# Performance work log

Measured on AMD Instinct MI355X. Metric: run time of the kernel, lower is better.

The kernel has to match this reference:

```python
import jax, jax.numpy as jnp
import numpy as np

B, N, H = 32, 2048, 128
L4H = 4 * H  # concatenated (c0,h0,c1,h1) embedding dim


def _lstm_cell(x, c, h, Wx, Wh, b):
    g = x @ Wx + h @ Wh + b                      # [B,N,4H]
    i, f, gg, o = jnp.split(g, 4, axis=-1)
    c_new = jax.nn.sigmoid(f) * c + jax.nn.sigmoid(i) * jnp.tanh(gg)
    h_new = jax.nn.sigmoid(o) * jnp.tanh(c_new)
    return c_new, h_new


def setup_inputs() -> dict:
    key = jax.random.key(0)
    ks = jax.random.split(key, 20)
    s = 0.05
    inp = {
        'node_embeddings': jax.random.normal(ks[0], (B, N, H), jnp.float32),
        'c0': jax.random.normal(ks[1], (B, N, H), jnp.float32),
        'h0': jax.random.normal(ks[2], (B, N, H), jnp.float32),
        'c1': jax.random.normal(ks[3], (B, N, H), jnp.float32),
        'h1': jax.random.normal(ks[4], (B, N, H), jnp.float32),
        'instruction_pointer': jax.random.uniform(ks[5], (B, N), jnp.float32),
        'Wx0': s * jax.random.normal(ks[6], (H, 4 * H), jnp.float32),
        'Wh0': s * jax.random.normal(ks[7], (H, 4 * H), jnp.float32),
        'b0': jnp.zeros((4 * H,), jnp.float32),
        'Wx1': s * jax.random.normal(ks[8], (H, 4 * H), jnp.float32),
        'Wh1': s * jax.random.normal(ks[9], (H, 4 * H), jnp.float32),
        'b1': jnp.zeros((4 * H,), jnp.float32),
        'raise_W': s * jax.random.normal(ks[10], (L4H, 2), jnp.float32),
        'raise_b': jnp.zeros((2,), jnp.float32),
        'branch_W': s * jax.random.normal(ks[11], (L4H, 2), jnp.float32),
        'branch_b': jnp.zeros((2,), jnp.float32),
        'true_indexes': jax.random.randint(ks[12], (B, N), 0, N, jnp.int32),
        'false_indexes': jax.random.randint(ks[13], (B, N), 0, N, jnp.int32),
        'raise_indexes': jax.random.randint(ks[14], (B, N), 0, N, jnp.int32),
        'exit_node_indexes': jax.random.randint(ks[15], (B,), 0, N, jnp.int32),
        'raise_node_indexes': jax.random.randint(ks[16], (B,), 0, N, jnp.int32),
        'current_step': jnp.zeros((B,), jnp.int32),
        'step_limits': jax.random.randint(ks[17], (B,), 1, 100, jnp.int32),
    }
    return inp


def reference(node_embeddings, c0, h0, c1, h1, instruction_pointer,
              Wx0, Wh0, b0, Wx1, Wh1, b1, raise_W, raise_b, branch_W, branch_b,
              true_indexes, false_indexes, raise_indexes,
              exit_node_indexes, raise_node_indexes, current_step, step_limits):
    num_nodes = node_embeddings.shape[1]

    # --- execute: stacked 2-layer LSTM per node (vectorized over B,N) ---
    c0n, h0n = _lstm_cell(node_embeddings, c0, h0, Wx0, Wh0, b0)
    c1n, h1n = _lstm_cell(h0n, c1, h1, Wx1, Wh1, b1)
    old = (c0, h0, c1, h1)
    contrib = (c0n, h0n, c1n, h1n)

    # --- mask exit and raise nodes: keep old hidden state there ---
    node_ids = jnp.arange(num_nodes)[None, :]                  # [1,N]
    m_exit = node_ids == exit_node_indexes[:, None]            # [B,N]
    m_raise = node_ids == raise_node_indexes[:, None]          # [B,N]
    m_keep = (m_exit | m_raise)[..., None]                     # raise_in_ipagnn=True
    contrib = tuple(jnp.where(m_keep, o, c) for o, c in zip(old, contrib))

    # --- raise / branch decisions ---
    emb = jnp.concatenate(contrib, axis=-1)                    # [B,N,4H]
    raise_dec = jax.nn.softmax(emb @ raise_W + raise_b, axis=-1)
    raise_dec = jnp.where(m_exit[..., None], jnp.array([0.0, 1.0], raise_dec.dtype), raise_dec)
    branch_dec = jax.nn.softmax(emb @ branch_W + branch_b, axis=-1)

    p_raise = raise_dec[..., 0]
    p_noraise = raise_dec[..., 1]
    p_true = p_noraise * branch_dec[..., 0]
    p_false = p_noraise * branch_dec[..., 1]

    seg = jax.vmap(lambda d, i: jax.ops.segment_sum(d, i, num_segments=num_nodes))

    # --- instruction pointer update (scatter-add over soft edges) ---
    ip = instruction_pointer
    ip_new = (seg(p_raise * ip, raise_indexes)
              + seg(p_true * ip, true_indexes)
              + seg(p_false * ip, false_indexes))               # [B,N]

    # --- hidden-state aggregation, weighted by instruction pointer ---
    denom = (ip_new + 1e-7)[..., None]                          # [B,N,1]
    wr = (p_raise * ip)[..., None]
    wt = (p_true * ip)[..., None]
    wf = (p_false * ip)[..., None]
    agg = tuple((seg(hc * wr, raise_indexes)
                 + seg(hc * wt, true_indexes)
                 + seg(hc * wf, false_indexes)) / denom
                for hc in contrib)

    # --- keep old state if example already hit its step limit ---
    live = (current_step < step_limits)                         # [B]
    ip_fin = jnp.where(live[:, None], ip_new, ip)
    hid_fin = tuple(jnp.where(live[:, None, None], a, o) for a, o in zip(agg, old))

    # pack carry: (c0,h0,c1,h1) embedding + instruction pointer -> [B,N,4H+1]
    return jnp.concatenate(list(hid_fin) + [ip_fin[..., None]], axis=-1)
```

## Files before the change

kernel.cpp:

```cpp
#include <hip/hip_runtime.h>
#include <hip/hip_bf16.h>

constexpr int Bc  = 32;
constexpr int Nc  = 2048;
constexpr int Hc  = 128;
constexpr int H4c = 512;
constexpr int BNc = Bc * Nc;

typedef __attribute__((ext_vector_type(8))) short short8;
typedef __attribute__((ext_vector_type(4))) float f32x4;

__device__ __forceinline__ float sigf(float x)  { return 1.f / (1.f + __expf(-x)); }
__device__ __forceinline__ float tanh_(float x) { return 1.f - 2.f / (__expf(2.f * x) + 1.f); }

__device__ __forceinline__ unsigned short bfu(float f) {
    union { float f; unsigned u; } a; a.f = f;
    unsigned u = a.u;
    return (unsigned short)((u + 0x7FFFu + ((u >> 16) & 1u)) >> 16);
}
__device__ __forceinline__ float bf2f(unsigned short u) {
    union { unsigned u; float f; } a; a.u = ((unsigned)u) << 16;
    return a.f;
}
__device__ __forceinline__ unsigned cvtpk(float lo, float hi) {
    unsigned r;
    asm("v_cvt_pk_bf16_f32 %0, %1, %2" : "=v"(r) : "v"(lo), "v"(hi));
    return r;
}

__device__ __forceinline__ int a_off(int buf, int row, int byte) {
    return buf * 5120 + row * 80 + byte;
}
__device__ __forceinline__ int cs_off(int row, int unit) {
    return row * 512 + ((unit ^ (row & 7)) << 4);
}

__global__ __launch_bounds__(256) void prep_kernel(
    const float* __restrict__ Wx0, const float* __restrict__ Wh0,
    const float* __restrict__ Wx1, const float* __restrict__ Wh1,
    unsigned short* __restrict__ W0F, unsigned short* __restrict__ W1F)
{
    int idx = blockIdx.x * 256 + threadIdx.x;
    int ct = idx >> 9, ks = (idx >> 6) & 7, lane = idx & 63;
    int col = ct * 16 + (lane & 15);
    unsigned short* p0 = W0F + (size_t)idx * 8;
    unsigned short* p1 = W1F + (size_t)idx * 8;
    #pragma unroll
    for (int e = 0; e < 8; ++e) {
        int k = ks * 32 + (lane >> 4) * 8 + e;
        float v0 = (k < 128) ? Wx0[k * 512 + col] : Wh0[(k - 128) * 512 + col];
        float v1 = (k < 128) ? Wx1[k * 512 + col] : Wh1[(k - 128) * 512 + col];
        p0[e] = bfu(v0);
        p1[e] = bfu(v1);
    }
}

__global__ __launch_bounds__(512, 4) void gemm0_kernel(
    const float* __restrict__ x_in,  const float* __restrict__ c0_in,
    const float* __restrict__ h0_in,
    const unsigned short* __restrict__ W0F, const float* __restrict__ b0,
    const int* __restrict__ exit_i, const int* __restrict__ raise_i,
    unsigned short* __restrict__ contrib)
{
    __shared__ __align__(16) char Ab[10240];
    __shared__ __align__(16) char Cs[32768];

    const int t    = threadIdx.x;
    const int w    = t >> 6, l = t & 63, lr = l & 15, lg = l >> 4;
    const int row0 = blockIdx.x * 64;
    const int bidx = row0 >> 11;
    const int eb   = exit_i[bidx];
    const int rbn  = raise_i[bidx];
    const int j    = w * 16 + lr;

    const int srow = t >> 3, sfq = t & 7;
#define STAGE0(c, bi)                                                          \
    {                                                                          \
        const float* sp = ((c) < 4 ? x_in : h0_in)                             \
            + (size_t)(row0 + srow) * Hc + ((c) & 3) * 32 + sfq * 4;           \
        float4 v = *(const float4*)sp;                                         \
        uint2 b2 = { cvtpk(v.x, v.y), cvtpk(v.z, v.w) };                       \
        *(uint2*)(Ab + a_off(bi, srow, sfq * 8)) = b2;                         \
    }

    f32x4 acc[4][4];
    #pragma unroll
    for (int g = 0; g < 4; ++g) {
        float bv = b0[g * 128 + j];
        f32x4 vv = {bv, bv, bv, bv};
        #pragma unroll
        for (int mt = 0; mt < 4; ++mt) acc[mt][g] = vv;
    }

    STAGE0(0, 0);
    short8 bn[4];
    #pragma unroll
    for (int g = 0; g < 4; ++g)
        bn[g] = *(const short8*)(W0F + ((size_t)((g * 8 + w) * 8) * 64 + l) * 8);
    #pragma unroll
    for (int c = 0; c < 8; ++c) {
        __syncthreads();
        short8 bc[4];
        #pragma unroll
        for (int g = 0; g < 4; ++g) bc[g] = bn[g];
        if (c < 7) {
            STAGE0(c + 1, (c + 1) & 1);
            #pragma unroll
            for (int g = 0; g < 4; ++g)
                bn[g] = *(const short8*)(W0F + ((size_t)((g * 8 + w) * 8 + c + 1) * 64 + l) * 8);
        }
        short8 a[4];
        #pragma unroll
        for (int mt = 0; mt < 4; ++mt)
            a[mt] = *(const short8*)(Ab + a_off(c & 1, mt * 16 + lr, lg * 16));
        #pragma unroll
        for (int mt = 0; mt < 4; ++mt)
            #pragma unroll
            for (int g = 0; g < 4; ++g)
                acc[mt][g] = __builtin_amdgcn_mfma_f32_16x16x32_bf16(
                    a[mt], bc[g], acc[mt][g], 0, 0, 0);
    }

    #pragma unroll
    for (int mt = 0; mt < 4; ++mt) {
        #pragma unroll
        for (int rr = 0; rr < 4; ++rr) {
            const int row  = mt * 16 + lg * 4 + rr;
            const int grow = row0 + row;
            const int n    = grow & (Nc - 1);
            float cold = c0_in[(size_t)grow * Hc + j];
            float ig = sigf(acc[mt][0][rr]);
            float fg = sigf(acc[mt][1][rr]);
            float gv = tanh_(acc[mt][2][rr]);
            float og = sigf(acc[mt][3][rr]);
            float cn = fg * cold + ig * gv;
            float hn = og * tanh_(cn);
            const bool keep = (n == eb) || (n == rbn);
            float cw = keep ? cold : cn;
            float hw = hn;
            if (keep) hw = h0_in[(size_t)grow * Hc + j];
            *(unsigned short*)(Cs + cs_off(row, j >> 3) + (j & 7) * 2)        = bfu(cw);
            *(unsigned short*)(Cs + cs_off(row, 16 + (j >> 3)) + (j & 7) * 2) = bfu(hw);
        }
    }
    __syncthreads();
    #pragma unroll
    for (int i = 0; i < 4; ++i) {
        const int idx = i * 512 + t;
        const int r = idx >> 5, u = idx & 31;
        short8 v = *(const short8*)(Cs + cs_off(r, u));
        *(short8*)(contrib + (size_t)(row0 + r) * H4c + u * 8) = v;
    }
#undef STAGE0
}

__global__ __launch_bounds__(512, 4) void gemm1_kernel(
    const unsigned short* __restrict__ contrib_r, const float* __restrict__ c1_in,
    const float* __restrict__ h1_in,
    const unsigned short* __restrict__ W1F, const float* __restrict__ b1,
    const float* __restrict__ rW, const float* __restrict__ rbv,
    const float* __restrict__ bW, const float* __restrict__ bbv,
    const float* __restrict__ ip_in,
    const int* __restrict__ exit_i, const int* __restrict__ raise_i,
    unsigned short* __restrict__ contrib, float* __restrict__ w_all)
{
    __shared__ __align__(16) char Ab[10240];
    __shared__ __align__(16) char Cs[32768];

    const int t    = threadIdx.x;
    const int w    = t >> 6, l = t & 63, lr = l & 15, lg = l >> 4;
    const int row0 = blockIdx.x * 64;
    const int bidx = row0 >> 11;
    const int eb   = exit_i[bidx];
    const int rbn  = raise_i[bidx];
    const int j    = w * 16 + lr;

    const int srow = t >> 3, sfq = t & 7;
#define STAGE1(c, bi)                                                          \
    {                                                                          \
        if ((c) < 4) {                                                         \
            ushort4 v = *(const ushort4*)(contrib_r                            \
                + (size_t)(row0 + srow) * H4c + 128 + ((c) & 3) * 32 + sfq * 4); \
            *(ushort4*)(Ab + a_off(bi, srow, sfq * 8)) = v;                    \
        } else {                                                               \
            const float* sp = h1_in + (size_t)(row0 + srow) * Hc               \
                + ((c) & 3) * 32 + sfq * 4;                                    \
            float4 v = *(const float4*)sp;                                     \
            uint2 b2 = { cvtpk(v.x, v.y), cvtpk(v.z, v.w) };                   \
            *(uint2*)(Ab + a_off(bi, srow, sfq * 8)) = b2;                     \
        }                                                                      \
    }

    f32x4 acc[4][4];
    #pragma unroll
    for (int g = 0; g < 4; ++g) {
        float bv = b1[g * 128 + j];
        f32x4 vv = {bv, bv, bv, bv};
        #pragma unroll
        for (int mt = 0; mt < 4; ++mt) acc[mt][g] = vv;
    }

    STAGE1(0, 0);
    short8 bn[4];
    #pragma unroll
    for (int g = 0; g < 4; ++g)
        bn[g] = *(const short8*)(W1F + ((size_t)((g * 8 + w) * 8) * 64 + l) * 8);
    #pragma unroll
    for (int c = 0; c < 8; ++c) {
        __syncthreads();
        short8 bc[4];
        #pragma unroll
        for (int g = 0; g < 4; ++g) bc[g] = bn[g];
        if (c < 7) {
            STAGE1(c + 1, (c + 1) & 1);
            #pragma unroll
            for (int g = 0; g < 4; ++g)
                bn[g] = *(const short8*)(W1F + ((size_t)((g * 8 + w) * 8 + c + 1) * 64 + l) * 8);
        }
        short8 a[4];
        #pragma unroll
        for (int mt = 0; mt < 4; ++mt)
            a[mt] = *(const short8*)(Ab + a_off(c & 1, mt * 16 + lr, lg * 16));
        #pragma unroll
        for (int mt = 0; mt < 4; ++mt)
            #pragma unroll
            for (int g = 0; g < 4; ++g)
                acc[mt][g] = __builtin_amdgcn_mfma_f32_16x16x32_bf16(
                    a[mt], bc[g], acc[mt][g], 0, 0, 0);
    }

    #pragma unroll
    for (int mt = 0; mt < 4; ++mt) {
        #pragma unroll
        for (int rr = 0; rr < 4; ++rr) {
            const int row  = mt * 16 + lg * 4 + rr;
            const int grow = row0 + row;
            const int n    = grow & (Nc - 1);
            float cold = c1_in[(size_t)grow * Hc + j];
            float ig = sigf(acc[mt][0][rr]);
            float fg = sigf(acc[mt][1][rr]);
            float gv = tanh_(acc[mt][2][rr]);
            float og = sigf(acc[mt][3][rr]);
            float cn = fg * cold + ig * gv;
            float hn = og * tanh_(cn);
            const bool keep = (n == eb) || (n == rbn);
            float cw = keep ? cold : cn;
            float hw = hn;
            if (keep) hw = h1_in[(size_t)grow * Hc + j];
            *(unsigned short*)(Cs + cs_off(row, j >> 3) + (j & 7) * 2)        = bfu(cw);
            *(unsigned short*)(Cs + cs_off(row, 16 + (j >> 3)) + (j & 7) * 2) = bfu(hw);
        }
    }
    __syncthreads();
    float* dw = (float*)Ab;
    if (t < 256) {
        ((float4*)dw)[t]       = ((const float4*)rW)[t];
        ((float4*)dw)[256 + t] = ((const float4*)bW)[t];
    }
    __syncthreads();
    #pragma unroll
    for (int i = 0; i < 4; ++i) {
        const int idx = i * 512 + t;
        const int r = idx >> 5, u = idx & 31;
        short8 v = *(const short8*)(Cs + cs_off(r, u));
        *(short8*)(contrib + (size_t)(row0 + r) * H4c + 256 + u * 8) = v;
    }

    {
        const int r8 = l >> 3, s = l & 7;
        const int row  = w * 8 + r8;
        const int grow = row0 + row;
        float pr0 = 0.f, pr1 = 0.f, pb0 = 0.f, pb1 = 0.f;
        #pragma unroll
        for (int cu = 0; cu < 8; ++cu) {
            short8 ev;
            if (s < 4)
                ev = *(const short8*)(contrib_r + (size_t)grow * H4c + s * 64 + cu * 8);
            else
                ev = *(const short8*)(Cs + cs_off(row, (s - 4) * 8 + cu));
            const int col0 = s * 64 + cu * 8;
            const float4* rp = (const float4*)(dw + col0 * 2);
            const float4* bp = (const float4*)(dw + 1024 + col0 * 2);
            #pragma unroll
            for (int q = 0; q < 4; ++q) {
                float4 rv = rp[q], bv = bp[q];
                float e0 = bf2f((unsigned short)ev[q * 2]);
                float e1 = bf2f((unsigned short)ev[q * 2 + 1]);
                pr0 += e0 * rv.x + e1 * rv.z;
                pr1 += e0 * rv.y + e1 * rv.w;
                pb0 += e0 * bv.x + e1 * bv.z;
                pb1 += e0 * bv.y + e1 * bv.w;
            }
        }
        #pragma unroll
        for (int m = 1; m < 8; m <<= 1) {
            pr0 += __shfl_xor(pr0, m);
            pr1 += __shfl_xor(pr1, m);
            pb0 += __shfl_xor(pb0, m);
            pb1 += __shfl_xor(pb1, m);
        }
        if (s == 0) {
            const int n = grow & (Nc - 1);
            float r0v = pr0 + rbv[0], r1v = pr1 + rbv[1];
            float m  = fmaxf(r0v, r1v);
            float z0 = __expf(r0v - m), z1 = __expf(r1v - m);
            float inv = 1.f / (z0 + z1);
            float praise = z0 * inv, pno = z1 * inv;
            if (n == eb) { praise = 0.f; pno = 1.f; }
            float q0 = pb0 + bbv[0], q1 = pb1 + bbv[1];
            float mm = fmaxf(q0, q1);
            float y0 = __expf(q0 - mm), y1 = __expf(q1 - mm);
            float binv = 1.f / (y0 + y1);
            float ipv = ip_in[grow];
            w_all[grow]            = praise * ipv;
            w_all[BNc + grow]      = pno * y0 * binv * ipv;
            w_all[2 * BNc + grow]  = pno * y1 * binv * ipv;
        }
    }
#undef STAGE1
}

__global__ __launch_bounds__(256) void build_kernel(
    const int* __restrict__ t_idx, const int* __restrict__ f_idx,
    const int* __restrict__ r_idx, int* __restrict__ head, int* __restrict__ nxt)
{
    const int row  = blockIdx.x * 256 + threadIdx.x;
    const int base = (row >> 11) << 11;
    const int e0 = row * 4;
    int o;
    o = atomicExch(&head[base + r_idx[row]], e0);     nxt[e0]     = o;
    o = atomicExch(&head[base + t_idx[row]], e0 + 1); nxt[e0 + 1] = o;
    o = atomicExch(&head[base + f_idx[row]], e0 + 2); nxt[e0 + 2] = o;
}

__global__ __launch_bounds__(256) void gather_kernel(
    const unsigned short* __restrict__ contrib, const float* __restrict__ w_all,
    const int* __restrict__ head, const int* __restrict__ nxt,
    const float* __restrict__ c0_in, const float* __restrict__ h0_in,
    const float* __restrict__ c1_in, const float* __restrict__ h1_in,
    const float* __restrict__ ip_in,
    const int* __restrict__ cstep, const int* __restrict__ slim,
    float* __restrict__ out)
{
    const int gtid = blockIdx.x * 256 + threadIdx.x;
    const int wid  = gtid >> 6;
    const int l    = gtid & 63;
    const int bidx = wid >> 11;

    float acc[8] = {0.f, 0.f, 0.f, 0.f, 0.f, 0.f, 0.f, 0.f};
    float ipsum = 0.f;

    int e = head[wid];
    while (e >= 0) {
        const int src = e >> 2;
        const float w = w_all[(e & 3) * BNc + src];
        const unsigned short* crow = contrib + (size_t)src * 512;
        #pragma unroll
        for (int q = 0; q < 8; ++q) acc[q] += w * bf2f(crow[q * 64 + l]);
        ipsum += w;
        e = nxt[e];
    }

    const bool live = cstep[bidx] < slim[bidx];
    float* orow = out + (size_t)wid * 513;
    if (live) {
        const float inv = 1.f / (ipsum + 1e-7f);
        #pragma unroll
        for (int q = 0; q < 8; ++q) orow[q * 64 + l] = acc[q] * inv;
        if (l == 0) orow[512] = ipsum;
    } else {
        #pragma unroll
        for (int q = 0; q < 8; ++q) {
            const int off = (q & 1) * 64 + l;
            const float* p = (q >> 1) == 0 ? c0_in : (q >> 1) == 1 ? h0_in
                           : (q >> 1) == 2 ? c1_in : h1_in;
            orow[q * 64 + l] = p[(size_t)wid * Hc + off];
        }
        if (l == 0) orow[512] = ip_in[wid];
    }
}

extern "C" void kernel_launch(void* const* d_in, const int* in_sizes, int n_in,
                              void* d_out, int out_size, void* d_ws, size_t ws_size,
                              hipStream_t stream) {
    const float* x     = (const float*)d_in[0];
    const float* c0    = (const float*)d_in[1];
    const float* h0    = (const float*)d_in[2];
    const float* c1    = (const float*)d_in[3];
    const float* h1    = (const float*)d_in[4];
    const float* ip    = (const float*)d_in[5];
    const float* Wx0   = (const float*)d_in[6];
    const float* Wh0   = (const float*)d_in[7];
    const float* b0    = (const float*)d_in[8];
    const float* Wx1   = (const float*)d_in[9];
    const float* Wh1   = (const float*)d_in[10];
    const float* b1    = (const float*)d_in[11];
    const float* rW    = (const float*)d_in[12];
    const float* rb    = (const float*)d_in[13];
    const float* bW    = (const float*)d_in[14];
    const float* bb    = (const float*)d_in[15];
    const int* t_idx   = (const int*)d_in[16];
    const int* f_idx   = (const int*)d_in[17];
    const int* r_idx   = (const int*)d_in[18];
    const int* exit_i  = (const int*)d_in[19];
    const int* raise_i = (const int*)d_in[20];
    const int* cstep   = (const int*)d_in[21];
    const int* slim    = (const int*)d_in[22];
    float* out = (float*)d_out;

    unsigned short* contrib = (unsigned short*)d_ws;
    unsigned short* W0F = contrib + (size_t)BNc * 512;
    unsigned short* W1F = W0F + 512 * 256;
    float* w_all = (float*)(W1F + 512 * 256);
    int*   head  = (int*)(w_all + 3 * (size_t)BNc);
    int*   nxt   = head + BNc;

    hipMemsetAsync(head, 0xFF, BNc * sizeof(int), stream);

    prep_kernel<<<64, 256, 0, stream>>>(Wx0, Wh0, Wx1, Wh1, W0F, W1F);
    gemm0_kernel<<<BNc / 64, 512, 0, stream>>>(x, c0, h0, W0F, b0,
                                               exit_i, raise_i, contrib);
    gemm1_kernel<<<BNc / 64, 512, 0, stream>>>(contrib, c1, h1, W1F, b1,
                                               rW, rb, bW, bb, ip,
                                               exit_i, raise_i, contrib, w_all);
    build_kernel<<<BNc / 256, 256, 0, stream>>>(t_idx, f_idx, r_idx, head, nxt);
    gather_kernel<<<BNc / 4, 256, 0, stream>>>(contrib, w_all, head, nxt,
                                               c0, h0, c1, h1, ip, cstep, slim, out);
}
```

Before: 199.6 us.

## Fuse both LSTM GEMM kernels and fold head memset into prep kernel

Merges the layer-0 and layer-1 GEMM kernels into one. The new h0 and the loaded h1 are kept in registers, packed to bf16 and written into shared memory, where they serve directly as the A operand of the second GEMM. This removes the global round trip of the layer-0 h output and drops one kernel launch. The head-list initialisation moves from a memset into prep_kernel, and build_kernel now runs before the GEMM. The cost is an extra 8 KB of shared memory per block and more live registers, which could lower occupancy.

```diff
diff --git a/kernel.cpp b/kernel.cpp
--- a/kernel.cpp
+++ b/kernel.cpp
@@ -38,9 +38,13 @@
 __global__ __launch_bounds__(256) void prep_kernel(
     const float* __restrict__ Wx0, const float* __restrict__ Wh0,
     const float* __restrict__ Wx1, const float* __restrict__ Wh1,
-    unsigned short* __restrict__ W0F, unsigned short* __restrict__ W1F)
+    unsigned short* __restrict__ W0F, unsigned short* __restrict__ W1F,
+    int* __restrict__ head)
 {
     int idx = blockIdx.x * 256 + threadIdx.x;
+    int4 m1 = { -1, -1, -1, -1 };
+    ((int4*)head)[idx] = m1;
+
     int ct = idx >> 9, ks = (idx >> 6) & 7, lane = idx & 63;
     int col = ct * 16 + (lane & 15);
     unsigned short* p0 = W0F + (size_t)idx * 8;
@@ -55,15 +59,21 @@
     }
 }
 
-__global__ __launch_bounds__(512, 4) void gemm0_kernel(
+__global__ __launch_bounds__(512, 4) void gemm_fused_kernel(
     const float* __restrict__ x_in,  const float* __restrict__ c0_in,
-    const float* __restrict__ h0_in,
-    const unsigned short* __restrict__ W0F, const float* __restrict__ b0,
+    const float* __restrict__ h0_in, const float* __restrict__ c1_in,
+    const float* __restrict__ h1_in,
+    const unsigned short* __restrict__ W0F, const unsigned short* __restrict__ W1F,
+    const float* __restrict__ b0, const float* __restrict__ b1,
+    const float* __restrict__ rW, const float* __restrict__ rbv,
+    const float* __restrict__ bW, const float* __restrict__ bbv,
+    const float* __restrict__ ip_in,
     const int* __restrict__ exit_i, const int* __restrict__ raise_i,
-    unsigned short* __restrict__ contrib)
+    unsigned short* __restrict__ contrib, float* __restrict__ w_all)
 {
     __shared__ __align__(16) char Ab[10240];
     __shared__ __align__(16) char Cs[32768];
+    __shared__ __align__(16) float dw[2048];
 
     const int t    = threadIdx.x;
     const int w    = t >> 6, l = t & 63, lr = l & 15, lg = l >> 4;
@@ -121,6 +131,7 @@
                     a[mt], bc[g], acc[mt][g], 0, 0, 0);
     }
 
+    unsigned hnp[4][4];
     #pragma unroll
     for (int mt = 0; mt < 4; ++mt) {
         #pragma unroll
@@ -129,6 +140,7 @@
             const int grow = row0 + row;
             const int n    = grow & (Nc - 1);
             float cold = c0_in[(size_t)grow * Hc + j];
+            float h1f  = h1_in[(size_t)grow * Hc + j];
             float ig = sigf(acc[mt][0][rr]);
             float fg = sigf(acc[mt][1][rr]);
             float gv = tanh_(acc[mt][2][rr]);
@@ -141,6 +153,7 @@
             if (keep) hw = h0_in[(size_t)grow * Hc + j];
             *(unsigned short*)(Cs + cs_off(row, j >> 3) + (j & 7) * 2)        = bfu(cw);
             *(unsigned short*)(Cs + cs_off(row, 16 + (j >> 3)) + (j & 7) * 2) = bfu(hw);
+            hnp[mt][rr] = cvtpk(hn, h1f);
         }
     }
     __syncthreads();
@@ -151,47 +164,24 @@
         short8 v = *(const short8*)(Cs + cs_off(r, u));
         *(short8*)(contrib + (size_t)(row0 + r) * H4c + u * 8) = v;
     }
-#undef STAGE0
-}
-
-__global__ __launch_bounds__(512, 4) void gemm1_kernel(
-    const unsigned short* __restrict__ contrib_r, const float* __restrict__ c1_in,
-    const float* __restrict__ h1_in,
-    const unsigned short* __restrict__ W1F, const float* __restrict__ b1,
-    const float* __restrict__ rW, const float* __restrict__ rbv,
-    const float* __restrict__ bW, const float* __restrict__ bbv,
-    const float* __restrict__ ip_in,
-    const int* __restrict__ exit_i, const int* __restrict__ raise_i,
-    unsigned short* __restrict__ contrib, float* __restrict__ w_all)
-{
-    __shared__ __align__(16) char Ab[10240];
-    __shared__ __align__(16) char Cs[32768];
-
-    const int t    = threadIdx.x;
-    const int w    = t >> 6, l = t & 63, lr = l & 15, lg = l >> 4;
-    const int row0 = blockIdx.x * 64;
-    const int bidx = row0 >> 11;
-    const int eb   = exit_i[bidx];
-    const int rbn  = raise_i[bidx];
-    const int j    = w * 16 + lr;
-
-    const int srow = t >> 3, sfq = t & 7;
-#define STAGE1(c, bi)                                                          \
-    {                                                                          \
-        if ((c) < 4) {                                                         \
-            ushort4 v = *(const ushort4*)(contrib_r                            \
-                + (size_t)(row0 + srow) * H4c + 128 + ((c) & 3) * 32 + sfq * 4); \
-            *(ushort4*)(Ab + a_off(bi, srow, sfq * 8)) = v;                    \
-        } else {                                                               \
-            const float* sp = h1_in + (size_t)(row0 + srow) * Hc               \
-                + ((c) & 3) * 32 + sfq * 4;                                    \
-            float4 v = *(const float4*)sp;                                     \
-            uint2 b2 = { cvtpk(v.x, v.y), cvtpk(v.z, v.w) };                   \
-            *(uint2*)(Ab + a_off(bi, srow, sfq * 8)) = b2;                     \
-        }                                                                      \
-    }
-
-    f32x4 acc[4][4];
+    __syncthreads();
+    #pragma unroll
+    for (int mt = 0; mt < 4; ++mt)
+        #pragma unroll
+        for (int rr = 0; rr < 4; ++rr) {
+            const int row = mt * 16 + lg * 4 + rr;
+            unsigned p = hnp[mt][rr];
+            *(unsigned short*)(Cs + cs_off(row, j >> 3) + (j & 7) * 2) =
+                (unsigned short)(p & 0xFFFFu);
+            *(unsigned short*)(Cs + cs_off(row, 16 + (j >> 3)) + (j & 7) * 2) =
+                (unsigned short)(p >> 16);
+        }
+    if (t < 256) {
+        ((float4*)dw)[t]       = ((const float4*)rW)[t];
+        ((float4*)dw)[256 + t] = ((const float4*)bW)[t];
+    }
+    __syncthreads();
+
     #pragma unroll
     for (int g = 0; g < 4; ++g) {
         float bv = b1[g * 128 + j];
@@ -199,28 +189,23 @@
         #pragma unroll
         for (int mt = 0; mt < 4; ++mt) acc[mt][g] = vv;
     }
-
-    STAGE1(0, 0);
-    short8 bn[4];
     #pragma unroll
     for (int g = 0; g < 4; ++g)
         bn[g] = *(const short8*)(W1F + ((size_t)((g * 8 + w) * 8) * 64 + l) * 8);
     #pragma unroll
-    for (int c = 0; c < 8; ++c) {
-        __syncthreads();
+    for (int ks = 0; ks < 8; ++ks) {
         short8 bc[4];
         #pragma unroll
         for (int g = 0; g < 4; ++g) bc[g] = bn[g];
-        if (c < 7) {
-            STAGE1(c + 1, (c + 1) & 1);
+        if (ks < 7) {
             #pragma unroll
             for (int g = 0; g < 4; ++g)
-                bn[g] = *(const short8*)(W1F + ((size_t)((g * 8 + w) * 8 + c + 1) * 64 + l) * 8);
+                bn[g] = *(const short8*)(W1F + ((size_t)((g * 8 + w) * 8 + ks + 1) * 64 + l) * 8);
         }
         short8 a[4];
         #pragma unroll
         for (int mt = 0; mt < 4; ++mt)
-            a[mt] = *(const short8*)(Ab + a_off(c & 1, mt * 16 + lr, lg * 16));
+            a[mt] = *(const short8*)(Cs + cs_off(mt * 16 + lr, ks * 4 + lg));
         #pragma unroll
         for (int mt = 0; mt < 4; ++mt)
             #pragma unroll
@@ -228,6 +213,7 @@
                 acc[mt][g] = __builtin_amdgcn_mfma_f32_16x16x32_bf16(
                     a[mt], bc[g], acc[mt][g], 0, 0, 0);
     }
+    __syncthreads();
 
     #pragma unroll
     for (int mt = 0; mt < 4; ++mt) {
@@ -252,12 +238,7 @@
         }
     }
     __syncthreads();
-    float* dw = (float*)Ab;
-    if (t < 256) {
-        ((float4*)dw)[t]       = ((const float4*)rW)[t];
-        ((float4*)dw)[256 + t] = ((const float4*)bW)[t];
-    }
-    __syncthreads();
+
     #pragma unroll
     for (int i = 0; i < 4; ++i) {
         const int idx = i * 512 + t;
@@ -275,7 +256,7 @@
         for (int cu = 0; cu < 8; ++cu) {
             short8 ev;
             if (s < 4)
-                ev = *(const short8*)(contrib_r + (size_t)grow * H4c + s * 64 + cu * 8);
+                ev = *(const short8*)(contrib + (size_t)grow * H4c + s * 64 + cu * 8);
             else
                 ev = *(const short8*)(Cs + cs_off(row, (s - 4) * 8 + cu));
             const int col0 = s * 64 + cu * 8;
@@ -317,7 +298,7 @@
             w_all[2 * BNc + grow]  = pno * y1 * binv * ipv;
         }
     }
-#undef STAGE1
+#undef STAGE0
 }
 
 __global__ __launch_bounds__(256) void build_kernel(
@@ -415,15 +396,12 @@
     int*   head  = (int*)(w_all + 3 * (size_t)BNc);
     int*   nxt   = head + BNc;
 
-    hipMemsetAsync(head, 0xFF, BNc * sizeof(int), stream);
-
-    prep_kernel<<<64, 256, 0, stream>>>(Wx0, Wh0, Wx1, Wh1, W0F, W1F);
-    gemm0_kernel<<<BNc / 64, 512, 0, stream>>>(x, c0, h0, W0F, b0,
-                                               exit_i, raise_i, contrib);
-    gemm1_kernel<<<BNc / 64, 512, 0, stream>>>(contrib, c1, h1, W1F, b1,
-                                               rW, rb, bW, bb, ip,
-                                               exit_i, raise_i, contrib, w_all);
+    prep_kernel<<<64, 256, 0, stream>>>(Wx0, Wh0, Wx1, Wh1, W0F, W1F, head);
     build_kernel<<<BNc / 256, 256, 0, stream>>>(t_idx, f_idx, r_idx, head, nxt);
+    gemm_fused_kernel<<<BNc / 64, 512, 0, stream>>>(x, c0, h0, c1, h1,
+                                                    W0F, W1F, b0, b1,
+                                                    rW, rb, bW, bb, ip,
+                                                    exit_i, raise_i, contrib, w_all);
     gather_kernel<<<BNc / 4, 256, 0, stream>>>(contrib, w_all, head, nxt,
                                                c0, h0, c1, h1, ip, cstep, slim, out);
 }
```

Measured after the change: 319.9 us. +60.2%, slower.
